# Performance work log

Measured on AMD Instinct MI355X. Metric: run time of the kernel, lower is better.

## Reference

```python
import jax, jax.numpy as jnp
import numpy as np
from jax import lax

VOCAB, ENC_DIM, PRED_H, JOINT_H = 4096, 1024, 640, 640
T, MAX_SYM, BLANK, SOS = 128, 30, 0, -1
S = T * (MAX_SYM + 1)  # upper bound on greedy-decode loop iterations


def setup_inputs() -> dict:
    key = jax.random.key(0)
    ks = jax.random.split(key, 10)
    rn = lambda k, shape, s: jax.random.normal(k, shape, jnp.float32) * s
    return {
        "enc_out": rn(ks[0], (1, T, ENC_DIM), 1.0),
        "out_len": T,
        "emb": rn(ks[1], (VOCAB, PRED_H), 0.1),
        "Wih0": rn(ks[2], (4 * PRED_H, PRED_H), 0.04),
        "Whh0": rn(ks[3], (4 * PRED_H, PRED_H), 0.04),
        "b0": jnp.zeros((4 * PRED_H,), jnp.float32),
        "Wih1": rn(ks[4], (4 * PRED_H, PRED_H), 0.04),
        "Whh1": rn(ks[5], (4 * PRED_H, PRED_H), 0.04),
        "b1": jnp.zeros((4 * PRED_H,), jnp.float32),
        "Wj1": rn(ks[6], (JOINT_H, ENC_DIM + PRED_H), 0.03),
        "bj1": jnp.zeros((JOINT_H,), jnp.float32),
        "Wj2": rn(ks[7], (VOCAB, JOINT_H), 0.04),
        "bj2": jnp.zeros((VOCAB,), jnp.float32),
    }


def _lstm_cell(x, h, c, Wih, Whh, b):
    z = x @ Wih.T + h @ Whh.T + b  # [4H], torch gate order i,f,g,o
    i, f, g, o = jnp.split(z, 4)
    c2 = jax.nn.sigmoid(f) * c + jax.nn.sigmoid(i) * jnp.tanh(g)
    return jax.nn.sigmoid(o) * jnp.tanh(c2), c2


def _decode(enc_out, timesteps, emb, Wih0, Whh0, b0, Wih1, Whh1, b1, Wj1, bj1, Wj2, bj2):
    enc = enc_out[0]  # [T, ENC_DIM]

    def step(carry, _):
        t, sa, last, h0, c0, h1, c1, labels, cnt, done = carry
        # prediction net step (SOS = -1 -> zero embedding)
        g_in = jnp.where(last < 0, 0.0, emb[jnp.maximum(last, 0)])
        h0n, c0n = _lstm_cell(g_in, h0, c0, Wih0, Whh0, b0)
        h1n, c1n = _lstm_cell(h0n, h1, c1, Wih1, Whh1, b1)
        # joint net on current encoder frame
        f = enc[jnp.minimum(t, T - 1)]
        hid = jax.nn.relu(Wj1 @ jnp.concatenate([f, h1n]) + bj1)
        logits = Wj2 @ hid + bj2  # [VOCAB]
        k = jnp.argmax(logits).astype(jnp.int32)
        stop_sym = (k == BLANK) | (sa >= MAX_SYM)
        emit = (~stop_sym) & (~done)
        adv = stop_sym & (~done)
        # emit: append symbol, keep hidden'; blank/max: advance time, discard hidden'
        last2 = jnp.where(emit, k, last)
        h0 = jnp.where(emit, h0n, h0); c0 = jnp.where(emit, c0n, c0)
        h1 = jnp.where(emit, h1n, h1); c1 = jnp.where(emit, c1n, c1)
        labels = labels.at[cnt].set(jnp.where(emit, k, labels[cnt]))
        cnt2 = cnt + emit.astype(jnp.int32)
        sa2 = jnp.where(emit, sa + 1, jnp.where(adv, 0, sa))
        t2 = t + adv.astype(jnp.int32)
        done2 = done | (adv & (t2 >= timesteps))
        out_logits = jnp.where(done, 0.0, logits)
        return (t2, sa2, last2, h0, c0, h1, c1, labels, cnt2, done2), out_logits

    zeros = jnp.zeros((PRED_H,), jnp.float32)
    carry0 = (jnp.int32(0), jnp.int32(0), jnp.int32(SOS),
              zeros, zeros, zeros, zeros,
              jnp.full((S,), -1, jnp.int32), jnp.int32(0), jnp.bool_(False))
    carry, logits_seq = lax.scan(step, carry0, None, length=S)
    labels, cnt = carry[7], carry[8]
    return logits_seq, labels, cnt


def reference(enc_out, out_len, emb, Wih0, Whh0, b0, Wih1, Whh1, b1, Wj1, bj1, Wj2, bj2):
    return _decode(enc_out, out_len, emb, Wih0, Whh0, b0, Wih1, Whh1, b1, Wj1, bj1, Wj2, bj2)
```

## Files before the change

### kernel.cpp

```cpp
#include <hip/hip_runtime.h>
#include <cmath>

#define VOCAB   4096
#define ENC_DIM 1024
#define PRED_H  640
#define JOINT_H 640
#define TMAX    128
#define MAX_SYM 30
#define NSTEPS  (TMAX*(MAX_SYM+1))
#define NWG     160
#define NTHR    512
#define RLX __ATOMIC_RELAXED
#define AGT __HIP_MEMORY_SCOPE_AGENT

typedef unsigned long long u64;
typedef __attribute__((ext_vector_type(4))) float f32x4;
typedef __attribute__((ext_vector_type(4))) unsigned int u32x4;


__device__ __forceinline__ float wave_red(float v){
  v += __shfl_xor(v, 32, 64);
  v += __shfl_xor(v, 16, 64);
  v += __shfl_xor(v,  8, 64);
  v += __shfl_xor(v,  4, 64);
  v += __shfl_xor(v,  2, 64);
  v += __shfl_xor(v,  1, 64);
  return v;
}

__device__ __forceinline__ float sigf(float x){ return 1.0f/(1.0f+expf(-x)); }

__device__ __forceinline__ void sendline(u64* base, int w, f32x4 hv, unsigned tag){
  u32x4 a, b;
  a.x = __float_as_uint(hv.x); a.y = tag; a.z = __float_as_uint(hv.y); a.w = tag;
  b.x = __float_as_uint(hv.z); b.y = tag; b.z = __float_as_uint(hv.w); b.w = tag;
  u64* p = base + ((size_t)w<<3);
  asm volatile("global_store_dwordx4 %0, %2, off sc0 sc1\n\t"
               "global_store_dwordx4 %1, %3, off sc0 sc1"
               :: "v"(p), "v"(p+2), "v"(a), "v"(b) : "memory");
}

__device__ __forceinline__ void pollline(const u64* base, float* dstLDS,
                                         unsigned tag, int i){
  const u64* p = base + ((size_t)i<<3);
  u32x4 v0, v1;
  for(;;){
    asm volatile("global_load_dwordx4 %0, %2, off sc0 sc1\n\t"
                 "global_load_dwordx4 %1, %3, off sc0 sc1\n\t"
                 "s_waitcnt vmcnt(0)"
                 : "=&v"(v0), "=&v"(v1) : "v"(p), "v"(p+2) : "memory");
    if (v0.y == tag && v0.w == tag && v1.y == tag && v1.w == tag) break;
    __builtin_amdgcn_s_sleep(1);
  }
  __builtin_amdgcn_sched_barrier(0);
  float* d = dstLDS + (i<<2);
  d[0] = __uint_as_float(v0.x);
  d[1] = __uint_as_float(v0.z);
  d[2] = __uint_as_float(v1.x);
  d[3] = __uint_as_float(v1.z);
}

__device__ __forceinline__ u64 mkentry(float lg, int r, unsigned ep){
  unsigned u = __float_as_uint(lg);
  u = (u & 0x80000000u) ? ~u : (u | 0x80000000u);
  return ((u64)u<<24) | ((u64)(ep&0xFFFu)<<12) | (u64)(4095 - r);
}

__global__ void init_ws(unsigned* ws){
  for (int i = threadIdx.x; i < 10240; i += 256) ws[i] = 0u;
}

__global__ __launch_bounds__(NTHR, 1)
void rnnt_decode(const float* __restrict__ enc,
                 const int*   __restrict__ outlen_p,
                 const float* __restrict__ emb,
                 const float* __restrict__ Wih0, const float* __restrict__ Whh0, const float* __restrict__ b0,
                 const float* __restrict__ Wih1, const float* __restrict__ Whh1, const float* __restrict__ b1,
                 const float* __restrict__ Wj1,  const float* __restrict__ bj1,
                 const float* __restrict__ Wj2,  const float* __restrict__ bj2,
                 float* __restrict__ out,
                 char* __restrict__ ws)
{
  const int wg = blockIdx.x, tid = threadIdx.x;
  const int wave = tid >> 6, lane = tid & 63;
  const int timesteps = outlen_p[0];

  u64* dataA = (u64*)(ws);
  u64* dataB = (u64*)(ws + 10240);
  u64* dataH = (u64*)(ws + 20480);
  u64* parts = (u64*)(ws + 30720);

  __shared__ float xsh[ENC_DIM];
  __shared__ float h0buf[PRED_H];
  __shared__ float h1buf[PRED_H];
  __shared__ float hidsh[JOINT_H];
  __shared__ float zsh[4][4];
  __shared__ float zjsA[8], zjsB[8];
  __shared__ float c0c[4], c1c[4], c0p[4], c1p[4];
  __shared__ float bj1sh[4];
  __shared__ u64 psh[8];
  __shared__ u64 pmx[3];

  const int jb = wg*4;
  const int pollid = tid - 256;
  const bool isPoll = ((unsigned)pollid < 160u);

  const int gA = wave & 3;
  const int jA = wave >> 2;
  const int rowA = gA*PRED_H + jb + jA;
  const int rowB = gA*PRED_H + jb + jA + 2;

  float w0xA[10], w0hA[10], w0xB[10], w0hB[10];
  float w1xA[10], w1hA[10], w1xB[10], w1hB[10];
  #pragma unroll
  for (int i = 0; i < 10; ++i){
    int c = lane + (i<<6);
    w0xA[i] = Wih0[(size_t)rowA*PRED_H + c];
    w0hA[i] = Whh0[(size_t)rowA*PRED_H + c];
    w1xA[i] = Wih1[(size_t)rowA*PRED_H + c];
    w1hA[i] = Whh1[(size_t)rowA*PRED_H + c];
    w0xB[i] = Wih0[(size_t)rowB*PRED_H + c];
    w0hB[i] = Whh0[(size_t)rowB*PRED_H + c];
    w1xB[i] = Wih1[(size_t)rowB*PRED_H + c];
    w1hB[i] = Whh1[(size_t)rowB*PRED_H + c];
  }
  const float bA0 = b0[rowA], bA1 = b1[rowA];
  const float bB0 = b0[rowB], bB1 = b1[rowB];

  const int grp = wave >> 2;
  const int vt  = ((wave & 3)<<6) | lane;
  const int rP0 = jb + grp;
  const int rP1 = jb + 2 + grp;
  float wjf0[4], wjh0[3], wjf1[4], wjh1[3];
  #pragma unroll
  for (int i = 0; i < 4; ++i){
    wjf0[i] = Wj1[(size_t)rP0*(ENC_DIM+PRED_H) + vt + (i<<8)];
    wjf1[i] = Wj1[(size_t)rP1*(ENC_DIM+PRED_H) + vt + (i<<8)];
  }
  #pragma unroll
  for (int i = 0; i < 3; ++i){
    int c = vt + (i<<8);
    wjh0[i] = (c < PRED_H) ? Wj1[(size_t)rP0*(ENC_DIM+PRED_H) + ENC_DIM + c] : 0.f;
    wjh1[i] = (c < PRED_H) ? Wj1[(size_t)rP1*(ENC_DIM+PRED_H) + ENC_DIM + c] : 0.f;
  }
  float ca0 = 0.f, ca1 = 0.f;

  const int nrows = (wg < 96) ? 26 : 25;
  const int r2b = wg*25 + (wg < 96 ? wg : 96);
  float wj2[4][10], bj2r[4];
  #pragma unroll
  for (int p = 0; p < 4; ++p){
    bool act = (p*8 + wave) < nrows;
    int r = act ? (r2b + p*8 + wave) : 0;
    #pragma unroll
    for (int i = 0; i < 10; ++i)
      wj2[p][i] = act ? Wj2[(size_t)r*JOINT_H + lane + (i<<6)] : 0.f;
    bj2r[p] = act ? bj2[r] : 0.f;
  }

  for (int i = tid; i < PRED_H; i += NTHR){ h0buf[i] = 0.f; h1buf[i] = 0.f; }
  if (tid < 4){ c0c[tid] = 0.f; c1c[tid] = 0.f; bj1sh[tid] = bj1[jb+tid]; }
  __syncthreads();

  int t = 0, sa = 0, last = -1, cnt = 0, tStaged = -1;
  bool done = false, reuse = false;
  float s0A = 0.f, s0B = 0.f, s1A = 0.f, s1B = 0.f;

  for (int s = 0; s < NSTEPS; ++s){
    if (done){
      if (wg < 8) out[(size_t)s*VOCAB + wg*NTHR + tid] = 0.f;
      continue;
    }
    const unsigned tag = (unsigned)(s + 1);

    if (!reuse){
      {
        float XA = 0.f, XB = 0.f;
        if (last >= 0){
          float xr[10];
          #pragma unroll
          for (int i = 0; i < 10; ++i)
            xr[i] = emb[(size_t)last*PRED_H + lane + (i<<6)];
          #pragma unroll
          for (int i = 0; i < 10; ++i){
            XA = fmaf(w0xA[i], xr[i], XA);
            XB = fmaf(w0xB[i], xr[i], XB);
          }
          XA = wave_red(XA);
          XB = wave_red(XB);
        }
        if (lane == 0){
          zsh[gA][jA]   = XA + s0A + bA0;
          zsh[gA][jA+2] = XB + s0B + bB0;
        }
      }
      __syncthreads();
      if (wave == 0){
        float hv = 0.f;
        if (lane < 4){
          float ig = sigf(zsh[0][lane]), fg = sigf(zsh[1][lane]);
          float gg = tanhf(zsh[2][lane]), og = sigf(zsh[3][lane]);
          float c2 = fg*c0c[lane] + ig*gg;
          c0p[lane] = c2;
          hv = og*tanhf(c2);
        }
        f32x4 v;
        v.x = __shfl(hv, 0, 64); v.y = __shfl(hv, 1, 64);
        v.z = __shfl(hv, 2, 64); v.w = __shfl(hv, 3, 64);
        if (lane == 0) sendline(dataA, wg, v, tag);
      }

      if (isPoll) pollline(dataA, h0buf, tag, pollid);
      __syncthreads();
      {
        float XA = 0.f, XB = 0.f;
        #pragma unroll
        for (int i = 0; i < 10; ++i){
          float h0 = h0buf[lane+(i<<6)];
          XA = fmaf(w1xA[i], h0, XA);
          XB = fmaf(w1xB[i], h0, XB);
        }
        XA = wave_red(XA);
        XB = wave_red(XB);
        if (lane == 0){
          zsh[gA][jA]   = XA + s1A + bA1;
          zsh[gA][jA+2] = XB + s1B + bB1;
        }
      }
      __syncthreads();
      if (wave == 0){
        float hv = 0.f;
        if (lane < 4){
          float ig = sigf(zsh[0][lane]), fg = sigf(zsh[1][lane]);
          float gg = tanhf(zsh[2][lane]), og = sigf(zsh[3][lane]);
          float c2 = fg*c1c[lane] + ig*gg;
          c1p[lane] = c2;
          hv = og*tanhf(c2);
        }
        f32x4 v;
        v.x = __shfl(hv, 0, 64); v.y = __shfl(hv, 1, 64);
        v.z = __shfl(hv, 2, 64); v.w = __shfl(hv, 3, 64);
        if (lane == 0) sendline(dataB, wg, v, tag);
      }
    }

    {
      int tcap = (t < TMAX-1) ? t : (TMAX-1);
      bool fNew = (tcap != tStaged);
      if (fNew)
        for (int i = tid; i < ENC_DIM; i += NTHR) xsh[i] = enc[(size_t)tcap*ENC_DIM + i];
      if (!reuse){
        if (isPoll) pollline(dataB, h1buf, tag, pollid);
      }
      __syncthreads();
      if (fNew){
        float a = 0.f, b = 0.f;
        #pragma unroll
        for (int i = 0; i < 4; ++i){
          a = fmaf(wjf0[i], xsh[vt+(i<<8)], a);
          b = fmaf(wjf1[i], xsh[vt+(i<<8)], b);
        }
        ca0 = a; ca1 = b;
        tStaged = tcap;
      }
      {
        float acc = ca0;
        #pragma unroll
        for (int i = 0; i < 3; ++i){
          int c = vt + (i<<8);
          acc = fmaf(wjh0[i], h1buf[(c < PRED_H) ? c : 0], acc);
        }
        acc = wave_red(acc);
        if (lane == 0) zjsA[wave] = acc;
        float acc2 = ca1;
        #pragma unroll
        for (int i = 0; i < 3; ++i){
          int c = vt + (i<<8);
          acc2 = fmaf(wjh1[i], h1buf[(c < PRED_H) ? c : 0], acc2);
        }
        acc2 = wave_red(acc2);
        if (lane == 0) zjsB[wave] = acc2;
      }
      __syncthreads();
      if (wave == 0){
        float hv = 0.f;
        if (lane < 4){
          float v;
          if (lane == 0)      v = zjsA[0]+zjsA[1]+zjsA[2]+zjsA[3] + bj1sh[0];
          else if (lane == 1) v = zjsA[4]+zjsA[5]+zjsA[6]+zjsA[7] + bj1sh[1];
          else if (lane == 2) v = zjsB[0]+zjsB[1]+zjsB[2]+zjsB[3] + bj1sh[2];
          else                v = zjsB[4]+zjsB[5]+zjsB[6]+zjsB[7] + bj1sh[3];
          hv = v > 0.f ? v : 0.f;
        }
        f32x4 v;
        v.x = __shfl(hv, 0, 64); v.y = __shfl(hv, 1, 64);
        v.z = __shfl(hv, 2, 64); v.w = __shfl(hv, 3, 64);
        if (lane == 0) sendline(dataH, wg, v, tag);
      }
    }

    int k;
    {
      if (isPoll) pollline(dataH, hidsh, tag, pollid);
      __syncthreads();
      {
        float a0 = 0.f, a1 = 0.f, a2 = 0.f, a3 = 0.f;
        #pragma unroll
        for (int i = 0; i < 10; ++i){
          float h = hidsh[lane+(i<<6)];
          a0 = fmaf(wj2[0][i], h, a0);
          a1 = fmaf(wj2[1][i], h, a1);
          a2 = fmaf(wj2[2][i], h, a2);
          a3 = fmaf(wj2[3][i], h, a3);
        }
        a0 = wave_red(a0); a1 = wave_red(a1);
        a2 = wave_red(a2); a3 = wave_red(a3);
        if (lane == 0){
          u64 best = 0;
          float av[4] = {a0, a1, a2, a3};
          #pragma unroll
          for (int p = 0; p < 4; ++p){
            if (p*8 + wave < nrows){
              int r = r2b + p*8 + wave;
              float lg = av[p] + bj2r[p];
              out[(size_t)s*VOCAB + r] = lg;
              u64 e = mkentry(lg, r, tag);
              if (e > best) best = e;
            }
          }
          psh[wave] = best;
        }
      }
      __syncthreads();
      if (tid == 0){
        u64 m = psh[0];
        #pragma unroll
        for (int w = 1; w < 8; ++w) if (psh[w] > m) m = psh[w];
        __hip_atomic_store(&parts[(size_t)wg<<3], m, RLX, AGT);
      }

      {
        float a0 = 0.f, b0v = 0.f, a1 = 0.f, b1v = 0.f;
        #pragma unroll
        for (int i = 0; i < 10; ++i){
          float h0p = h0buf[lane+(i<<6)];
          float h1p = h1buf[lane+(i<<6)];
          a0  = fmaf(w0hA[i], h0p, a0);
          b0v = fmaf(w0hB[i], h0p, b0v);
          a1  = fmaf(w1hA[i], h1p, a1);
          b1v = fmaf(w1hB[i], h1p, b1v);
        }
        s0A = wave_red(a0);  s0B = wave_red(b0v);
        s1A = wave_red(a1);  s1B = wave_red(b1v);
      }

      u64 myp = 0;
      if (tid < 160){
        for(;;){
          u64 e = __hip_atomic_load(&parts[(size_t)tid<<3], RLX, AGT);
          if ((unsigned)((e>>12) & 0xFFFu) == (tag & 0xFFFu)){ myp = e; break; }
          __builtin_amdgcn_s_sleep(1);
        }
      }
      if (wave < 3){
        #pragma unroll
        for (int off = 32; off; off >>= 1){
          u64 o = __shfl_xor(myp, off, 64);
          if (o > myp) myp = o;
        }
        if (lane == 0) pmx[wave] = myp;
      }
      __syncthreads();
      u64 m = pmx[0];
      if (pmx[1] > m) m = pmx[1];
      if (pmx[2] > m) m = pmx[2];
      k = 4095 - (int)(m & 0xFFFull);
    }

    bool stop = (k == 0) || (sa >= MAX_SYM);
    if (!stop){
      if (wg == 0 && tid == 0) out[(size_t)NSTEPS*VOCAB + cnt] = (float)k;
      if (tid < 4){ c0c[tid] = c0p[tid]; c1c[tid] = c1p[tid]; }
      cnt++; sa++; last = k; reuse = false;
    } else {
      sa = 0; t++; reuse = true;
      if (t >= timesteps) done = true;
    }
  }

  size_t lab = (size_t)NSTEPS*VOCAB;
  int gidx = wg*NTHR + tid;
  for (int i = cnt + gidx; i < NSTEPS; i += NWG*NTHR) out[lab + i] = -1.f;
  if (wg == 0 && tid == 0) out[lab + NSTEPS] = (float)cnt;
}

extern "C" void kernel_launch(void* const* d_in, const int* in_sizes, int n_in,
                              void* d_out, int out_size, void* d_ws, size_t ws_size,
                              hipStream_t stream) {
  const float* enc  = (const float*)d_in[0];
  const int*   olen = (const int*)  d_in[1];
  const float* emb  = (const float*)d_in[2];
  const float* Wih0 = (const float*)d_in[3];
  const float* Whh0 = (const float*)d_in[4];
  const float* b0   = (const float*)d_in[5];
  const float* Wih1 = (const float*)d_in[6];
  const float* Whh1 = (const float*)d_in[7];
  const float* b1   = (const float*)d_in[8];
  const float* Wj1  = (const float*)d_in[9];
  const float* bj1  = (const float*)d_in[10];
  const float* Wj2  = (const float*)d_in[11];
  const float* bj2  = (const float*)d_in[12];
  float* out = (float*)d_out;
  char* ws = (char*)d_ws;

  init_ws<<<1, 256, 0, stream>>>((unsigned*)d_ws);

  void* args[] = {&enc,&olen,&emb,&Wih0,&Whh0,&b0,&Wih1,&Whh1,&b1,
                  &Wj1,&bj1,&Wj2,&bj2,&out,&ws};
  hipLaunchCooperativeKernel((const void*)rnnt_decode, dim3(NWG), dim3(NTHR),
                             args, 0, stream);
}
```

Before: 41.03 ms.

## Replace intra-block __syncthreads with tagged LDS spin-waits for reductions

Several __syncthreads barriers in the per-step decode loop are replaced by tagged 64-bit LDS slots. Consumer waves spin on these slots until every value carries the current step tag, so producers never wait on a full block barrier. The LSTM cell states move from shared memory into registers of wave 0. This aims to cut block-wide barrier latency on the sequential critical path, but adds LDS atomic polling and relies on the memory ordering of relaxed workgroup-scope atomics.

```diff
diff --git a/kernel.cpp b/kernel.cpp
--- a/kernel.cpp
+++ b/kernel.cpp
@@ -12,6 +12,7 @@
 #define NTHR    512
 #define RLX __ATOMIC_RELAXED
 #define AGT __HIP_MEMORY_SCOPE_AGENT
+#define WGS __HIP_MEMORY_SCOPE_WORKGROUP
 
 typedef unsigned long long u64;
 typedef __attribute__((ext_vector_type(4))) float f32x4;
@@ -64,6 +65,26 @@
   unsigned u = __float_as_uint(lg);
   u = (u & 0x80000000u) ? ~u : (u | 0x80000000u);
   return ((u64)u<<24) | ((u64)(ep&0xFFFu)<<12) | (u64)(4095 - r);
+}
+
+__device__ __forceinline__ void ltstore(u64* p, float v, unsigned tag){
+  __hip_atomic_store(p, ((u64)tag<<32) | (u64)__float_as_uint(v), RLX, WGS);
+}
+__device__ __forceinline__ void lspin4(u64* t, int base, int stride,
+                                       unsigned tag, float z[4]){
+  for(;;){
+    u64 a = __hip_atomic_load(&t[base],          RLX, WGS);
+    u64 b = __hip_atomic_load(&t[base+stride],   RLX, WGS);
+    u64 c = __hip_atomic_load(&t[base+2*stride], RLX, WGS);
+    u64 d = __hip_atomic_load(&t[base+3*stride], RLX, WGS);
+    if (((unsigned)(a>>32)==tag) & ((unsigned)(b>>32)==tag) &
+        ((unsigned)(c>>32)==tag) & ((unsigned)(d>>32)==tag)){
+      z[0]=__uint_as_float((unsigned)a); z[1]=__uint_as_float((unsigned)b);
+      z[2]=__uint_as_float((unsigned)c); z[3]=__uint_as_float((unsigned)d);
+      return;
+    }
+    __builtin_amdgcn_s_sleep(1);
+  }
 }
 
 __global__ void init_ws(unsigned* ws){
@@ -94,12 +115,12 @@
   __shared__ float h0buf[PRED_H];
   __shared__ float h1buf[PRED_H];
   __shared__ float hidsh[JOINT_H];
-  __shared__ float zsh[4][4];
-  __shared__ float zjsA[8], zjsB[8];
-  __shared__ float c0c[4], c1c[4], c0p[4], c1p[4];
+  __shared__ u64 zshT0[16];
+  __shared__ u64 zshT1[16];
+  __shared__ u64 zjsT[16];
+  __shared__ u64 pshT[8];
+  __shared__ u64 pmxT[3];
   __shared__ float bj1sh[4];
-  __shared__ u64 psh[8];
-  __shared__ u64 pmx[3];
 
   const int jb = wg*4;
   const int pollid = tid - 256;
@@ -159,12 +180,16 @@
   }
 
   for (int i = tid; i < PRED_H; i += NTHR){ h0buf[i] = 0.f; h1buf[i] = 0.f; }
-  if (tid < 4){ c0c[tid] = 0.f; c1c[tid] = 0.f; bj1sh[tid] = bj1[jb+tid]; }
+  if (tid < 16){ zshT0[tid] = 0; zshT1[tid] = 0; zjsT[tid] = 0; }
+  if (tid < 8) pshT[tid] = 0;
+  if (tid < 3) pmxT[tid] = 0;
+  if (tid < 4) bj1sh[tid] = bj1[jb+tid];
   __syncthreads();
 
   int t = 0, sa = 0, last = -1, cnt = 0, tStaged = -1;
   bool done = false, reuse = false;
   float s0A = 0.f, s0B = 0.f, s1A = 0.f, s1B = 0.f;
+  float c0c_r = 0.f, c1c_r = 0.f, c0p_r = 0.f, c1p_r = 0.f;
 
   for (int s = 0; s < NSTEPS; ++s){
     if (done){
@@ -190,18 +215,19 @@
           XB = wave_red(XB);
         }
         if (lane == 0){
-          zsh[gA][jA]   = XA + s0A + bA0;
-          zsh[gA][jA+2] = XB + s0B + bB0;
-        }
-      }
-      __syncthreads();
+          ltstore(&zshT0[gA*4+jA],   XA + s0A + bA0, tag);
+          ltstore(&zshT0[gA*4+jA+2], XB + s0B + bB0, tag);
+        }
+      }
       if (wave == 0){
         float hv = 0.f;
         if (lane < 4){
-          float ig = sigf(zsh[0][lane]), fg = sigf(zsh[1][lane]);
-          float gg = tanhf(zsh[2][lane]), og = sigf(zsh[3][lane]);
-          float c2 = fg*c0c[lane] + ig*gg;
-          c0p[lane] = c2;
+          float z[4];
+          lspin4(zshT0, lane, 4, tag, z);
+          float ig = sigf(z[0]), fg = sigf(z[1]);
+          float gg = tanhf(z[2]), og = sigf(z[3]);
+          float c2 = fg*c0c_r + ig*gg;
+          c0p_r = c2;
           hv = og*tanhf(c2);
         }
         f32x4 v;
@@ -223,18 +249,19 @@
         XA = wave_red(XA);
         XB = wave_red(XB);
         if (lane == 0){
-          zsh[gA][jA]   = XA + s1A + bA1;
-          zsh[gA][jA+2] = XB + s1B + bB1;
-        }
-      }
-      __syncthreads();
+          ltstore(&zshT1[gA*4+jA],   XA + s1A + bA1, tag);
+          ltstore(&zshT1[gA*4+jA+2], XB + s1B + bB1, tag);
+        }
+      }
       if (wave == 0){
         float hv = 0.f;
         if (lane < 4){
-          float ig = sigf(zsh[0][lane]), fg = sigf(zsh[1][lane]);
-          float gg = tanhf(zsh[2][lane]), og = sigf(zsh[3][lane]);
-          float c2 = fg*c1c[lane] + ig*gg;
-          c1p[lane] = c2;
+          float z[4];
+          lspin4(zshT1, lane, 4, tag, z);
+          float ig = sigf(z[0]), fg = sigf(z[1]);
+          float gg = tanhf(z[2]), og = sigf(z[3]);
+          float c2 = fg*c1c_r + ig*gg;
+          c1p_r = c2;
           hv = og*tanhf(c2);
         }
         f32x4 v;
@@ -271,7 +298,6 @@
           acc = fmaf(wjh0[i], h1buf[(c < PRED_H) ? c : 0], acc);
         }
         acc = wave_red(acc);
-        if (lane == 0) zjsA[wave] = acc;
         float acc2 = ca1;
         #pragma unroll
         for (int i = 0; i < 3; ++i){
@@ -279,17 +305,17 @@
           acc2 = fmaf(wjh1[i], h1buf[(c < PRED_H) ? c : 0], acc2);
         }
         acc2 = wave_red(acc2);
-        if (lane == 0) zjsB[wave] = acc2;
-      }
-      __syncthreads();
+        if (lane == 0){
+          ltstore(&zjsT[wave],   acc,  tag);
+          ltstore(&zjsT[8+wave], acc2, tag);
+        }
+      }
       if (wave == 0){
         float hv = 0.f;
         if (lane < 4){
-          float v;
-          if (lane == 0)      v = zjsA[0]+zjsA[1]+zjsA[2]+zjsA[3] + bj1sh[0];
-          else if (lane == 1) v = zjsA[4]+zjsA[5]+zjsA[6]+zjsA[7] + bj1sh[1];
-          else if (lane == 2) v = zjsB[0]+zjsB[1]+zjsB[2]+zjsB[3] + bj1sh[2];
-          else                v = zjsB[4]+zjsB[5]+zjsB[6]+zjsB[7] + bj1sh[3];
+          float z[4];
+          lspin4(zjsT, lane*4, 1, tag, z);
+          float v = z[0]+z[1]+z[2]+z[3] + bj1sh[lane];
           hv = v > 0.f ? v : 0.f;
         }
         f32x4 v;
@@ -328,14 +354,18 @@
               if (e > best) best = e;
             }
           }
-          psh[wave] = best;
-        }
-      }
-      __syncthreads();
+          __hip_atomic_store(&pshT[wave], best, RLX, WGS);
+        }
+      }
       if (tid == 0){
-        u64 m = psh[0];
-        #pragma unroll
-        for (int w = 1; w < 8; ++w) if (psh[w] > m) m = psh[w];
+        u64 m = 0;
+        #pragma unroll
+        for (int w = 0; w < 8; ++w){
+          u64 e;
+          do { e = __hip_atomic_load(&pshT[w], RLX, WGS); }
+          while ((unsigned)((e>>12) & 0xFFFu) != (tag & 0xFFFu));
+          if (e > m) m = e;
+        }
         __hip_atomic_store(&parts[(size_t)wg<<3], m, RLX, AGT);
       }
 
@@ -368,19 +398,28 @@
           u64 o = __shfl_xor(myp, off, 64);
           if (o > myp) myp = o;
         }
-        if (lane == 0) pmx[wave] = myp;
-      }
-      __syncthreads();
-      u64 m = pmx[0];
-      if (pmx[1] > m) m = pmx[1];
-      if (pmx[2] > m) m = pmx[2];
+        if (lane == 0) __hip_atomic_store(&pmxT[wave], myp, RLX, WGS);
+      }
+      u64 m0, m1, m2;
+      const unsigned t12 = tag & 0xFFFu;
+      for(;;){
+        m0 = __hip_atomic_load(&pmxT[0], RLX, WGS);
+        m1 = __hip_atomic_load(&pmxT[1], RLX, WGS);
+        m2 = __hip_atomic_load(&pmxT[2], RLX, WGS);
+        if ((((unsigned)(m0>>12)&0xFFFu)==t12) & (((unsigned)(m1>>12)&0xFFFu)==t12) &
+            (((unsigned)(m2>>12)&0xFFFu)==t12)) break;
+        __builtin_amdgcn_s_sleep(1);
+      }
+      u64 m = m0;
+      if (m1 > m) m = m1;
+      if (m2 > m) m = m2;
       k = 4095 - (int)(m & 0xFFFull);
     }
 
     bool stop = (k == 0) || (sa >= MAX_SYM);
     if (!stop){
       if (wg == 0 && tid == 0) out[(size_t)NSTEPS*VOCAB + cnt] = (float)k;
-      if (tid < 4){ c0c[tid] = c0p[tid]; c1c[tid] = c1p[tid]; }
+      if (wave == 0 && lane < 4){ c0c_r = c0p_r; c1c_r = c1p_r; }
       cnt++; sa++; last = k; reuse = false;
     } else {
       sa = 0; t++; reuse = true;
```

After: 44.28 ms. 1.08x slower.
